# Kernel tuning notes

Measured on AMD Instinct MI355X. Metric: run time of the kernel, lower is better.

## Reference

```python
import jax, jax.numpy as jnp
import numpy as np

EPS = 1e-5
TEMPERATURE = 1.0


def _gn(x, w, b):
    # GroupNorm(dim, dim): num_groups == channels -> per-channel norm over spatial
    mu = x.mean((2, 3), keepdims=True)
    var = x.var((2, 3), keepdims=True)
    return (x - mu) * jax.lax.rsqrt(var + EPS) * w[None, :, None, None] + b[None, :, None, None]


def _deconv(x, w, b):
    # torch ConvTranspose2d(Cin, Cout, 3, stride=2, padding=1, output_padding=1)
    # == dilated conv with lhs_dilation=2, padding (1,2); kernel flip absorbed into random weights
    y = jax.lax.conv_general_dilated(
        x, w, window_strides=(1, 1), padding=((1, 2), (1, 2)),
        lhs_dilation=(2, 2), dimension_numbers=('NCHW', 'OIHW', 'NCHW'))
    return y + b[None, :, None, None]


def _spatial_softmax(logits, temp):
    # logits (..., h, w) -> expected (x, y) coords in [-1, 1], shape (..., 2)
    h, w = logits.shape[-2], logits.shape[-1]
    p = jax.nn.softmax(logits.reshape(*logits.shape[:-2], h * w) / temp, axis=-1)
    ys, xs = jnp.meshgrid(jnp.linspace(-1.0, 1.0, h), jnp.linspace(-1.0, 1.0, w), indexing='ij')
    ex = p @ xs.reshape(-1)
    ey = p @ ys.reshape(-1)
    return jnp.stack([ex, ey], axis=-1)


def setup_inputs() -> dict:
    key = jax.random.key(0)
    ks = iter(jax.random.split(key, 40))
    B, FC, FH = 512, 256, 4   # batch, encoder channels, encoder spatial
    H = 512                   # hidden_size
    STEPS, NHEADS, C = 5, 3, H // 8

    def nrm(shape, scale):
        return jax.random.normal(next(ks), shape, jnp.float32) * scale

    inp = {
        'feat': nrm((B, FC, FH, FH), 1.0),
        'action': jax.random.randint(next(ks), (B,), 0, NHEADS),
        'scene_idx': jax.random.randint(next(ks), (B,), 0, 10),
        'fc_w': nrm((FC, H), (2.0 / FC) ** 0.5),
        'fc_b': jnp.zeros((H,), jnp.float32),
    }
    for i, d in enumerate([512, 256, 128]):
        inp[f'gw{i}'] = jnp.ones((d,), jnp.float32)
        inp[f'gb{i}'] = jnp.zeros((d,), jnp.float32)
        inp[f'dw{i}'] = nrm((d // 2, d, 3, 3), (2.0 / (d * 9)) ** 0.5)
        inp[f'db{i}'] = jnp.zeros((d // 2,), jnp.float32)
    inp['hgw'] = jnp.ones((NHEADS, C), jnp.float32)
    inp['hgb'] = jnp.zeros((NHEADS, C), jnp.float32)
    inp['hcw'] = nrm((NHEADS, STEPS, C), (2.0 / C) ** 0.5)
    inp['hcb'] = jnp.zeros((NHEADS, STEPS), jnp.float32)
    return inp


def reference(feat, action, scene_idx, fc_w, fc_b,
              gw0, gb0, dw0, db0, gw1, gb1, dw1, db1, gw2, gb2, dw2, db2,
              hgw, hgb, hcw, hcb):
    # visual_fc1 applied channel-last == 1x1 linear over channels
    x = jax.nn.relu(jnp.einsum('bchw,cd->bdhw', feat, fc_w) + fc_b[None, :, None, None])
    # deconv stack: (B,512,4,4) -> (B,256,8,8) -> (B,128,16,16) -> (B,64,32,32)
    for gw, gb, dw, db in ((gw0, gb0, dw0, db0), (gw1, gb1, dw1, db1), (gw2, gb2, dw2, db2)):
        x = jax.nn.relu(_deconv(_gn(x, gw, gb), dw, db))
    # expert heads: shared per-channel normalization, head-specific affine fused into 1x1 conv
    mu = x.mean((2, 3), keepdims=True)
    var = x.var((2, 3), keepdims=True)
    xn = (x - mu) * jax.lax.rsqrt(var + EPS)                       # (B,64,32,32)
    w_eff = hcw * hgw[:, None, :]                                  # (A,S,C)
    b_eff = hcb + jnp.einsum('asc,ac->as', hcw, hgb)               # (A,S)
    logits = jnp.einsum('bchw,asc->abshw', xn, w_eff) + b_eff[:, None, :, None, None]
    coords = _spatial_softmax(logits, TEMPERATURE)                 # (A,B,S,2)
    # route each sample to its action's head (== masked scatter loop in torch)
    out = coords[action, jnp.arange(action.shape[0])]              # (B,S,2)
    return out
```

## Files before the change

### kernel.cpp

```cpp
#include <hip/hip_runtime.h>
#include <hip/hip_bf16.h>

#define DI __device__ __forceinline__
using u16 = unsigned short;
using u32 = unsigned int;

typedef short short8 __attribute__((ext_vector_type(8)));
typedef float f32x4 __attribute__((ext_vector_type(4)));

#define F4C(v, i) ((i) == 0 ? (v).x : (i) == 1 ? (v).y : (i) == 2 ? (v).z : (v).w)

DI float bflo(u32 u) { return __uint_as_float(u << 16); }
DI float bfhi(u32 u) { return __uint_as_float(u & 0xffff0000u); }
DI u16 f2bf(float a) {
  u32 xu = __float_as_uint(a);
  return (u16)((xu + 0x7fffu + ((xu >> 16) & 1)) >> 16);
}
DI u32 pack_bf16x2(float a, float b) {
  u32 xu = __float_as_uint(a), yu = __float_as_uint(b);
  xu = (xu + 0x7fffu + ((xu >> 16) & 1)) >> 16;
  yu = (yu + 0x7fffu + ((yu >> 16) & 1)) >> 16;
  return (xu & 0xffffu) | (yu << 16);
}

static constexpr size_t OFF_REGB = 0;
static constexpr size_t OFF_REGA = 16777216;
static constexpr size_t OFF_WT0  = 33554432;
static constexpr size_t OFF_WT1  = OFF_WT0 + 1179648;
static constexpr size_t OFF_WT2  = OFF_WT1 + 294912;
static constexpr size_t OFF_WTF  = OFF_WT2 + 73728;
static constexpr size_t OFF_ST   = 35200000;
static constexpr size_t O_PSUM = OFF_ST + 1048576;

__global__ __launch_bounds__(256)
void wtrans_all(const float* __restrict__ dw0, const float* __restrict__ dw1,
                const float* __restrict__ dw2, const float* __restrict__ fcw,
                u16* __restrict__ wt0, u16* __restrict__ wt1,
                u16* __restrict__ wt2, u16* __restrict__ wtf)
{
  int id = blockIdx.x * 256 + threadIdx.x;
  if (id < 131072) {
    int m = id >> 9, c = id & 511;
    const float* src = dw0 + ((size_t)m * 512 + c) * 9;
#pragma unroll
    for (int tap = 0; tap < 9; ++tap)
      wt0[((size_t)tap * 256 + m) * 512 + c] = f2bf(src[tap]);
  } else if (id < 163840) {
    int j = id - 131072;
    int m = j >> 8, c = j & 255;
    const float* src = dw1 + ((size_t)m * 256 + c) * 9;
#pragma unroll
    for (int tap = 0; tap < 9; ++tap)
      wt1[((size_t)tap * 128 + m) * 256 + c] = f2bf(src[tap]);
  } else if (id < 172032) {
    int j = id - 163840;
    int m = j >> 7, c = j & 127;
    const float* src = dw2 + ((size_t)m * 128 + c) * 9;
#pragma unroll
    for (int tap = 0; tap < 9; ++tap)
      wt2[((size_t)tap * 64 + m) * 128 + c] = f2bf(src[tap]);
  } else {
    int j = id - 172032;
    int d = j >> 8, c = j & 255;
    wtf[j] = f2bf(fcw[c * 512 + d]);
  }
}

DI void fc_stage_A(const float* __restrict__ feat, int b, u16* Ab, int t)
{
#pragma unroll
  for (int it = 0; it < 2; ++it) {
    int idx = t + it * 256;
    int cp = idx >> 2, hw4 = idx & 3;
    int c = cp * 2;
    const float* xp = feat + ((size_t)b * 256 + c) * 16 + hw4 * 4;
    float4 v0 = *(const float4*)xp;
    float4 v1 = *(const float4*)(xp + 16);
    int c64 = c >> 6, jb = (c & 63) >> 3;
#pragma unroll
    for (int j = 0; j < 4; ++j) {
      int hw = hw4 * 4 + j;
      int row = c64 * 16 + hw;
      *(u32*)&Ab[(row << 6) + ((jb ^ (row & 7)) << 3) + (c & 7)] =
          pack_bf16x2(F4C(v0, j), F4C(v1, j));
    }
  }
}

__global__ __launch_bounds__(256, 2)
void fc_mfma(const float* __restrict__ feat, const u16* __restrict__ wtf,
             const float* __restrict__ fb, const float* __restrict__ gw,
             const float* __restrict__ gb, u16* __restrict__ x0)
{
  __shared__ __align__(16) u16 Wl[256 * 64];
  __shared__ __align__(16) u16 Al[2][64 * 64];
  const int t = threadIdx.x;
  const int lane = t & 63, wave = t >> 6;
  const int n15 = lane & 15, kq = lane >> 4;
  const int d0 = blockIdx.x * 64;
  const int b0 = blockIdx.y * 8;

#pragma unroll
  for (int it = 0; it < 8; ++it) {
    int idx = t + it * 256;
    int dl = idx >> 5, jb32 = idx & 31;
    int row = (jb32 >> 3) * 64 + dl, jb = jb32 & 7;
    uint4 v = *(const uint4*)(wtf + (size_t)(d0 + dl) * 256 + jb32 * 8);
    *(uint4*)&Wl[(row << 6) + ((jb ^ (row & 7)) << 3)] = v;
  }
  fc_stage_A(feat, b0, Al[0], t);

  const int dg = d0 + wave * 16 + n15;
  const float bvn = fb[dg];
  const float gwv = gw[dg], gbv = gb[dg];

  for (int bi = 0; bi < 8; ++bi) {
    __syncthreads();
    if (bi + 1 < 8) fc_stage_A(feat, b0 + bi + 1, Al[(bi + 1) & 1], t);

    const u16* A = Al[bi & 1];
    f32x4 acc0 = {0.f, 0.f, 0.f, 0.f}, acc1 = {0.f, 0.f, 0.f, 0.f};
#pragma unroll
    for (int ks = 0; ks < 8; ++ks) {
      int js = ks * 4 + kq;
      int ra = (js >> 3) * 16 + n15;
      int rb = (js >> 3) * 64 + wave * 16 + n15;
      short8 av = *(const short8*)&A[(ra << 6) + (((js & 7) ^ (ra & 7)) << 3)];
      short8 bv = *(const short8*)&Wl[(rb << 6) + (((js & 7) ^ (rb & 7)) << 3)];
      if (ks & 1) acc1 = __builtin_amdgcn_mfma_f32_16x16x32_bf16(av, bv, acc1, 0, 0, 0);
      else        acc0 = __builtin_amdgcn_mfma_f32_16x16x32_bf16(av, bv, acc0, 0, 0, 0);
    }

    int b = b0 + bi;
    float v[4], s = 0.f, s2 = 0.f;
#pragma unroll
    for (int r = 0; r < 4; ++r) {
      v[r] = fmaxf(acc0[r] + acc1[r] + bvn, 0.f);
      s += v[r]; s2 += v[r] * v[r];
    }
    s  += __shfl_xor(s, 16, 64);  s  += __shfl_xor(s, 32, 64);
    s2 += __shfl_xor(s2, 16, 64); s2 += __shfl_xor(s2, 32, 64);
    float mu = s * (1.f / 16.f);
    float var = fmaxf(s2 * (1.f / 16.f) - mu * mu, 0.f);
    float scale = gwv * rsqrtf(var + 1e-5f);
    float shift = gbv - mu * scale;
#pragma unroll
    for (int r = 0; r < 4; ++r) v[r] = v[r] * scale + shift;
    uint2 pk = {pack_bf16x2(v[0], v[1]), pack_bf16x2(v[2], v[3])};
    *(uint2*)&x0[((size_t)b * 512 + dg) * 16 + kq * 4] = pk;
  }
}

template<int STAGE>
__global__ __launch_bounds__(256, 3)
void deconv_mfma(const u16* __restrict__ x, const u16* __restrict__ wt,
                 const float* __restrict__ bias, u16* __restrict__ y,
                 const float* __restrict__ gwn, const float* __restrict__ gbn)
{
  constexpr int CI  = STAGE == 0 ? 512 : 256;
  constexpr int CO  = CI / 2;
  constexpr int H   = STAGE == 0 ? 4 : 8;
  constexpr int S2I = H * H, S2O = 4 * S2I, W2 = 2 * H;
  constexpr int WP  = H + 1;
  constexpr int XROWS = STAGE == 0 ? 100 : 81;
  constexpr int NCH = CI / 64;
  __shared__ __align__(16) u16 Wl[288 * 64];
  __shared__ __align__(16) u16 Xl[XROWS * 64];
  __shared__ float2 sbuf[2][2][16];
  __shared__ float scl[32], shl[32];

  const int t = threadIdx.x;
  const int lane = t & 63, wave = t >> 6;
  const int ms = wave >> 1, ns = wave & 1;
  const int n15 = lane & 15, kq = lane >> 4;

  int m0, b0;
  m0 = blockIdx.x * 32; b0 = (STAGE == 0) ? blockIdx.y * 4 : blockIdx.y;

  int xrow[2];
#pragma unroll
  for (int ni = 0; ni < 2; ++ni) {
    if constexpr (STAGE == 0) xrow[ni] = (ns * 2 + ni) * 25 + (n15 >> 2) * 5 + (n15 & 3);
    else                      xrow[ni] = (2 * (ns * 2 + ni) + (n15 >> 3)) * 9 + (n15 & 7);
  }
  const int am = ms * 16 + n15;

  for (int i = t; i < XROWS * 32; i += 256) ((u32*)Xl)[i] = 0;

  f32x4 acc[2][4];
#pragma unroll
  for (int ni = 0; ni < 2; ++ni)
#pragma unroll
    for (int c = 0; c < 4; ++c) acc[ni][c] = f32x4{0.f, 0.f, 0.f, 0.f};

  for (int ch = 0; ch < NCH; ++ch) {
    const int c0 = ch * 64;
    __syncthreads();

#pragma unroll
    for (int it = 0; it < 9; ++it) {
      int idx = t + it * 256;
      int row = idx >> 3, jb = idx & 7;
      int tap = row >> 5, ml = row & 31;
      uint4 v = *(const uint4*)(wt + ((size_t)(tap * CO + m0 + ml)) * CI + c0 + jb * 8);
      *(uint4*)&Wl[(row << 6) + ((jb ^ (row & 7)) << 3)] = v;
    }

    for (int idx = t; idx < 16 * 32; idx += 256) {
      int q = idx & 15, p = idx >> 4;
      int c = c0 + 2 * p;
      int b, ldr, gpos;
      if constexpr (STAGE == 0) {
        int img = q >> 2, iy = q & 3;
        b = b0 + img; gpos = iy * 4; ldr = img * 25 + iy * 5;
      } else {
        int iy = q >> 1, cq = q & 1;
        b = b0; gpos = iy * 8 + cq * 4; ldr = iy * 9 + cq * 4;
      }
      const u16* xp = x + ((size_t)b * CI + c) * S2I + gpos;
      uint2 q0 = *(const uint2*)xp;
      uint2 q1 = *(const uint2*)(xp + S2I);
      int jb = p >> 2, sub = p & 3;
#pragma unroll
      for (int j = 0; j < 4; ++j) {
        int row = ldr + j;
        u32 w0 = (j < 2) ? q0.x : q0.y;
        u32 w1 = (j < 2) ? q1.x : q1.y;
        u32 lo = (j & 1) ? (w0 >> 16) : (w0 & 0xffffu);
        u32 hi = (j & 1) ? (w1 & 0xffff0000u) : (w1 << 16);
        *(u32*)&Xl[(row << 6) + ((jb ^ (row & 7)) << 3) + sub * 2] = lo | hi;
      }
    }
    __syncthreads();

#pragma unroll
    for (int s = 0; s < 2; ++s) {
      const int js = s * 4 + kq;
      short8 a[9];
#pragma unroll
      for (int tap = 0; tap < 9; ++tap) {
        int row = tap * 32 + am;
        a[tap] = *(const short8*)&Wl[(row << 6) + ((js ^ (row & 7)) << 3)];
      }
#pragma unroll
      for (int ni = 0; ni < 2; ++ni) {
        int r0 = xrow[ni], r1 = r0 + 1, r2 = r0 + WP, r3 = r0 + WP + 1;
        short8 b00 = *(const short8*)&Xl[(r0 << 6) + ((js ^ (r0 & 7)) << 3)];
        short8 b01 = *(const short8*)&Xl[(r1 << 6) + ((js ^ (r1 & 7)) << 3)];
        short8 b10 = *(const short8*)&Xl[(r2 << 6) + ((js ^ (r2 & 7)) << 3)];
        short8 b11 = *(const short8*)&Xl[(r3 << 6) + ((js ^ (r3 & 7)) << 3)];
        acc[ni][0] = __builtin_amdgcn_mfma_f32_16x16x32_bf16(a[4], b00, acc[ni][0], 0, 0, 0);
        acc[ni][1] = __builtin_amdgcn_mfma_f32_16x16x32_bf16(a[3], b00, acc[ni][1], 0, 0, 0);
        acc[ni][1] = __builtin_amdgcn_mfma_f32_16x16x32_bf16(a[5], b01, acc[ni][1], 0, 0, 0);
        acc[ni][2] = __builtin_amdgcn_mfma_f32_16x16x32_bf16(a[1], b00, acc[ni][2], 0, 0, 0);
        acc[ni][2] = __builtin_amdgcn_mfma_f32_16x16x32_bf16(a[7], b10, acc[ni][2], 0, 0, 0);
        acc[ni][3] = __builtin_amdgcn_mfma_f32_16x16x32_bf16(a[0], b00, acc[ni][3], 0, 0, 0);
        acc[ni][3] = __builtin_amdgcn_mfma_f32_16x16x32_bf16(a[2], b01, acc[ni][3], 0, 0, 0);
        acc[ni][3] = __builtin_amdgcn_mfma_f32_16x16x32_bf16(a[6], b10, acc[ni][3], 0, 0, 0);
        acc[ni][3] = __builtin_amdgcn_mfma_f32_16x16x32_bf16(a[8], b11, acc[ni][3], 0, 0, 0);
      }
    }
  }

  float bv[4];
#pragma unroll
  for (int r = 0; r < 4; ++r) bv[r] = bias[m0 + ms * 16 + kq * 4 + r];

  if constexpr (STAGE == 0) {
    float gw4[4], gb4[4];
#pragma unroll
    for (int r = 0; r < 4; ++r) {
      int m = m0 + ms * 16 + kq * 4 + r;
      gw4[r] = gwn[m]; gb4[r] = gbn[m];
    }
#pragma unroll
    for (int ni = 0; ni < 2; ++ni) {
      int b = b0 + ns * 2 + ni, iy = n15 >> 2, ix = n15 & 3;
      float val[4][4];
      float sr[4] = {0.f, 0.f, 0.f, 0.f}, sr2[4] = {0.f, 0.f, 0.f, 0.f};
#pragma unroll
      for (int cl = 0; cl < 4; ++cl)
#pragma unroll
        for (int r = 0; r < 4; ++r) {
          val[cl][r] = fmaxf(acc[ni][cl][r] + bv[r], 0.f);
          sr[r] += val[cl][r]; sr2[r] += val[cl][r] * val[cl][r];
        }
#pragma unroll
      for (int r = 0; r < 4; ++r) {
#pragma unroll
        for (int off = 1; off <= 8; off <<= 1) {
          sr[r]  += __shfl_xor(sr[r], off, 64);
          sr2[r] += __shfl_xor(sr2[r], off, 64);
        }
      }
      float scv[4], shv[4];
#pragma unroll
      for (int r = 0; r < 4; ++r) {
        float mu = sr[r] * (1.f / 64.f);
        float var = fmaxf(sr2[r] * (1.f / 64.f) - mu * mu, 0.f);
        scv[r] = gw4[r] * rsqrtf(var + 1e-5f);
        shv[r] = gb4[r] - mu * scv[r];
      }
#pragma unroll
      for (int r = 0; r < 4; ++r) {
        int m = m0 + ms * 16 + kq * 4 + r;
        size_t base = ((size_t)b * CO + m) * S2O + (size_t)(2 * iy) * W2 + 2 * ix;
        *(u32*)(y + base)      = pack_bf16x2(val[0][r] * scv[r] + shv[r],
                                             val[1][r] * scv[r] + shv[r]);
        *(u32*)(y + base + W2) = pack_bf16x2(val[2][r] * scv[r] + shv[r],
                                             val[3][r] * scv[r] + shv[r]);
      }
    }
  } else {
    float sr[4] = {0.f, 0.f, 0.f, 0.f}, sr2[4] = {0.f, 0.f, 0.f, 0.f};
#pragma unroll
    for (int ni = 0; ni < 2; ++ni)
#pragma unroll
      for (int cl = 0; cl < 4; ++cl)
#pragma unroll
        for (int r = 0; r < 4; ++r) {
          float v = fmaxf(acc[ni][cl][r] + bv[r], 0.f);
          sr[r] += v; sr2[r] += v * v;
        }
#pragma unroll
    for (int r = 0; r < 4; ++r) {
#pragma unroll
      for (int off = 1; off <= 8; off <<= 1) {
        sr[r]  += __shfl_xor(sr[r], off, 64);
        sr2[r] += __shfl_xor(sr2[r], off, 64);
      }
    }
    __syncthreads();
    if (n15 == 0) {
#pragma unroll
      for (int r = 0; r < 4; ++r) sbuf[ms][ns][kq * 4 + r] = float2{sr[r], sr2[r]};
    }
    __syncthreads();
    if (t < 32) {
      int msx = t >> 4, i = t & 15;
      float2 p0 = sbuf[msx][0][i], p1 = sbuf[msx][1][i];
      float s = p0.x + p1.x, s2 = p0.y + p1.y;
      float mu = s * (1.f / 256.f);
      float var = fmaxf(s2 * (1.f / 256.f) - mu * mu, 0.f);
      int m = m0 + msx * 16 + i;
      float scale = gwn[m] * rsqrtf(var + 1e-5f);
      scl[t] = scale;
      shl[t] = gbn[m] - mu * scale;
    }
    __syncthreads();
    float scv[4], shv[4];
#pragma unroll
    for (int r = 0; r < 4; ++r) {
      scv[r] = scl[ms * 16 + kq * 4 + r];
      shv[r] = shl[ms * 16 + kq * 4 + r];
    }
#pragma unroll
    for (int ni = 0; ni < 2; ++ni) {
      int iy = 2 * (ns * 2 + ni) + (n15 >> 3), ix = n15 & 7;
#pragma unroll
      for (int cl = 0; cl < 4; ++cl) {
        int opx = (2 * iy + (cl >> 1)) * 16 + 2 * ix + (cl & 1);
        size_t base = ((size_t)b0 * 256 + opx) * 128 + m0 + ms * 16 + kq * 4;
        float v0 = fmaxf(acc[ni][cl][0] + bv[0], 0.f) * scv[0] + shv[0];
        float v1 = fmaxf(acc[ni][cl][1] + bv[1], 0.f) * scv[1] + shv[1];
        float v2 = fmaxf(acc[ni][cl][2] + bv[2], 0.f) * scv[2] + shv[2];
        float v3 = fmaxf(acc[ni][cl][3] + bv[3], 0.f) * scv[3] + shv[3];
        *(u32*)(y + base)     = pack_bf16x2(v0, v1);
        *(u32*)(y + base + 2) = pack_bf16x2(v2, v3);
      }
    }
  }
}

#define XRD(row) (*(const short8*)&Xl[((row) << 6) + (((js ^ ((row) & 7))) << 3)])
__global__ __launch_bounds__(256, 2)
void deconv2_q(const u16* __restrict__ x, const u16* __restrict__ wt,
               const float* __restrict__ bias, u16* __restrict__ y,
               float2* __restrict__ psum)
{
  __shared__ __align__(16) u16 Wl[288 * 64];
  __shared__ __align__(16) u16 Xl[153 * 64];
  __shared__ float2 sbuf[2][2][16];

  const int t = threadIdx.x;
  const int lane = t & 63, wave = t >> 6;
  const int ms = wave >> 1, ns = wave & 1;
  const int n15 = lane & 15, kq = lane >> 4;
  const int m0  = (blockIdx.x & 1) * 32;
  const int qz2 = blockIdx.x >> 1;
  const int b   = blockIdx.y;

  for (int i = t; i < 153 * 32; i += 256) ((u32*)Xl)[i] = 0;

  const int am = ms * 16 + n15;
  const int xr0 = (ns * 4) * 17 + n15;

  f32x4 acc[4][4];
#pragma unroll
  for (int ni = 0; ni < 4; ++ni)
#pragma unroll
    for (int c = 0; c < 4; ++c) acc[ni][c] = f32x4{0.f, 0.f, 0.f, 0.f};

  const int NPX = (qz2 == 0) ? 144 : 128;
  for (int ch = 0; ch < 2; ++ch) {
    const int c0 = ch * 64;
    __syncthreads();

#pragma unroll
    for (int it = 0; it < 9; ++it) {
      int idx = t + it * 256;
      int row = idx >> 3, jb = idx & 7;
      int tap = row >> 5, ml = row & 31;
      uint4 v = *(const uint4*)(wt + ((size_t)(tap * 64 + m0 + ml)) * 128 + c0 + jb * 8);
      *(uint4*)&Wl[(row << 6) + ((jb ^ (row & 7)) << 3)] = v;
    }

    for (int idx = t; idx < NPX * 8; idx += 256) {
      int pxl = idx >> 3, jb = idx & 7;
      int rl = pxl >> 4, ix = pxl & 15;
      int gpx = (8 * qz2 + rl) * 16 + ix;
      uint4 q = *(const uint4*)(x + ((size_t)b * 256 + gpx) * 128 + c0 + jb * 8);
      int row = rl * 17 + ix;
      *(uint4*)&Xl[(row << 6) + ((jb ^ (row & 7)) << 3)] = q;
    }
    __syncthreads();

#pragma unroll
    for (int s = 0; s < 2; ++s) {
      const int js = s * 4 + kq;
      short8 a[9];
#pragma unroll
      for (int tap = 0; tap < 9; ++tap) {
        int row = tap * 32 + am;
        a[tap] = *(const short8*)&Wl[(row << 6) + ((js ^ (row & 7)) << 3)];
      }
      short8 Brow[10];
#pragma unroll
      for (int k = 0; k < 5; ++k) {
        Brow[2 * k]     = XRD(xr0 + 17 * k);
        Brow[2 * k + 1] = XRD(xr0 + 17 * k + 1);
      }
      __builtin_amdgcn_s_setprio(1);
#pragma unroll
      for (int ni = 0; ni < 4; ++ni) {
        short8 b00 = Brow[2 * ni],     b01 = Brow[2 * ni + 1];
        short8 b10 = Brow[2 * ni + 2], b11 = Brow[2 * ni + 3];
        acc[ni][0] = __builtin_amdgcn_mfma_f32_16x16x32_bf16(a[4], b00, acc[ni][0], 0, 0, 0);
        acc[ni][1] = __builtin_amdgcn_mfma_f32_16x16x32_bf16(a[3], b00, acc[ni][1], 0, 0, 0);
        acc[ni][1] = __builtin_amdgcn_mfma_f32_16x16x32_bf16(a[5], b01, acc[ni][1], 0, 0, 0);
        acc[ni][2] = __builtin_amdgcn_mfma_f32_16x16x32_bf16(a[1], b00, acc[ni][2], 0, 0, 0);
        acc[ni][2] = __builtin_amdgcn_mfma_f32_16x16x32_bf16(a[7], b10, acc[ni][2], 0, 0, 0);
        acc[ni][3] = __builtin_amdgcn_mfma_f32_16x16x32_bf16(a[0], b00, acc[ni][3], 0, 0, 0);
        acc[ni][3] = __builtin_amdgcn_mfma_f32_16x16x32_bf16(a[2], b01, acc[ni][3], 0, 0, 0);
        acc[ni][3] = __builtin_amdgcn_mfma_f32_16x16x32_bf16(a[6], b10, acc[ni][3], 0, 0, 0);
        acc[ni][3] = __builtin_amdgcn_mfma_f32_16x16x32_bf16(a[8], b11, acc[ni][3], 0, 0, 0);
      }
      __builtin_amdgcn_s_setprio(0);
    }
  }

  float bv[4];
#pragma unroll
  for (int r = 0; r < 4; ++r) bv[r] = bias[m0 + ms * 16 + kq * 4 + r];
  float sr[4] = {0.f, 0.f, 0.f, 0.f}, sr2[4] = {0.f, 0.f, 0.f, 0.f};
#pragma unroll
  for (int ni = 0; ni < 4; ++ni) {
    int iy = 8 * qz2 + ns * 4 + ni, ix = n15;
#pragma unroll
    for (int r = 0; r < 4; ++r) {
      int m = m0 + ms * 16 + kq * 4 + r;
      float v00 = fmaxf(acc[ni][0][r] + bv[r], 0.f);
      float v01 = fmaxf(acc[ni][1][r] + bv[r], 0.f);
      float v10 = fmaxf(acc[ni][2][r] + bv[r], 0.f);
      float v11 = fmaxf(acc[ni][3][r] + bv[r], 0.f);
      size_t base = ((size_t)b * 64 + m) * 1024 + (size_t)(2 * iy) * 32 + 2 * ix;
      *(u32*)(y + base)      = pack_bf16x2(v00, v01);
      *(u32*)(y + base + 32) = pack_bf16x2(v10, v11);
      sr[r]  += v00 + v01 + v10 + v11;
      sr2[r] += v00 * v00 + v01 * v01 + v10 * v10 + v11 * v11;
    }
  }
#pragma unroll
  for (int r = 0; r < 4; ++r) {
#pragma unroll
    for (int off = 1; off <= 8; off <<= 1) {
      sr[r]  += __shfl_xor(sr[r], off, 64);
      sr2[r] += __shfl_xor(sr2[r], off, 64);
    }
  }
  __syncthreads();
  if (n15 == 0) {
#pragma unroll
    for (int r = 0; r < 4; ++r) sbuf[ms][ns][kq * 4 + r] = float2{sr[r], sr2[r]};
  }
  __syncthreads();
  if (t < 32) {
    int msx = t >> 4, i = t & 15;
    float2 p0 = sbuf[msx][0][i], p1 = sbuf[msx][1][i];
    int m = m0 + msx * 16 + i;
    psum[((size_t)b * 64 + m) * 2 + qz2] = float2{p0.x + p1.x, p0.y + p1.y};
  }
}

DI float breduce_sum(float v, float* buf) {
#pragma unroll
  for (int off = 32; off; off >>= 1) v += __shfl_xor(v, off, 64);
  if ((threadIdx.x & 63) == 0) buf[threadIdx.x >> 6] = v;
  __syncthreads();
  float r = (buf[0] + buf[1]) + (buf[2] + buf[3]);
  __syncthreads();
  return r;
}
DI float breduce_max(float v, float* buf) {
#pragma unroll
  for (int off = 32; off; off >>= 1) v = fmaxf(v, __shfl_xor(v, off, 64));
  if ((threadIdx.x & 63) == 0) buf[threadIdx.x >> 6] = v;
  __syncthreads();
  float r = fmaxf(fmaxf(buf[0], buf[1]), fmaxf(buf[2], buf[3]));
  __syncthreads();
  return r;
}

__global__ __launch_bounds__(256)
void head_kernel(const u16* __restrict__ x3, const float2* __restrict__ psum,
                 const int* __restrict__ action, const float* __restrict__ hgw,
                 const float* __restrict__ hcw, float* __restrict__ out)
{
  constexpr int C = 64, S = 5, P = 1024;
  const int b = blockIdx.x, t = threadIdx.x;
  const int a = action[b];
  __shared__ float weff[S * C];
  __shared__ float sc_l[C], sh_l[C];
  __shared__ float rbuf[4];
  if (t < C) {
    float2 p0 = psum[((size_t)b * C + t) * 2 + 0];
    float2 p1 = psum[((size_t)b * C + t) * 2 + 1];
    float s = p0.x + p1.x, s2 = p0.y + p1.y;
    float mu = s * (1.f / 1024.f);
    float var = fmaxf(s2 * (1.f / 1024.f) - mu * mu, 0.f);
    float rstd = rsqrtf(var + 1e-5f);
    sc_l[t] = rstd; sh_l[t] = -mu * rstd;
  }
  for (int j = t; j < S * C; j += 256) {
    int s = j >> 6, c = j & 63;
    weff[j] = hcw[(a * S + s) * C + c] * hgw[a * C + c];
  }
  __syncthreads();

  float L[S][4];
#pragma unroll
  for (int s = 0; s < S; ++s)
#pragma unroll
    for (int k = 0; k < 4; ++k) L[s][k] = 0.f;

  const u32* xb = (const u32*)(x3 + (size_t)b * C * P);
  for (int c = 0; c < C; ++c) {
    float scv = sc_l[c], shv = sh_l[c];
    u32 u0 = xb[c * 512 + t];
    u32 u1 = xb[c * 512 + t + 256];
    float xv[4] = {bflo(u0) * scv + shv, bfhi(u0) * scv + shv,
                   bflo(u1) * scv + shv, bfhi(u1) * scv + shv};
#pragma unroll
    for (int s = 0; s < S; ++s) {
      float wv = weff[s * C + c];
#pragma unroll
      for (int k = 0; k < 4; ++k) L[s][k] += xv[k] * wv;
    }
  }

#pragma unroll
  for (int s = 0; s < S; ++s) {
    float m = fmaxf(fmaxf(L[s][0], L[s][1]), fmaxf(L[s][2], L[s][3]));
    m = breduce_max(m, rbuf);
    float se = 0.f, sx = 0.f, sy = 0.f;
    const int pix[4] = {2 * t, 2 * t + 1, 512 + 2 * t, 512 + 2 * t + 1};
#pragma unroll
    for (int k = 0; k < 4; ++k) {
      int p = pix[k];
      float e = __expf(L[s][k] - m);
      se += e;
      sx += e * ((float)(p & 31) * (2.f / 31.f) - 1.f);
      sy += e * ((float)(p >> 5) * (2.f / 31.f) - 1.f);
    }
    se = breduce_sum(se, rbuf);
    sx = breduce_sum(sx, rbuf);
    sy = breduce_sum(sy, rbuf);
    if (t == 0) {
      out[(b * S + s) * 2 + 0] = sx / se;
      out[(b * S + s) * 2 + 1] = sy / se;
    }
  }
}

extern "C" void kernel_launch(void* const* d_in, const int* in_sizes, int n_in,
                              void* d_out, int out_size, void* d_ws, size_t ws_size,
                              hipStream_t stream)
{
  (void)in_sizes; (void)n_in; (void)out_size; (void)ws_size;
  const float* feat   = (const float*)d_in[0];
  const int*   action = (const int*)d_in[1];
  const float* fc_w = (const float*)d_in[3];
  const float* fc_b = (const float*)d_in[4];
  const float* gw0  = (const float*)d_in[5];
  const float* gb0  = (const float*)d_in[6];
  const float* dw0  = (const float*)d_in[7];
  const float* db0  = (const float*)d_in[8];
  const float* gw1  = (const float*)d_in[9];
  const float* gb1  = (const float*)d_in[10];
  const float* dw1  = (const float*)d_in[11];
  const float* db1  = (const float*)d_in[12];
  const float* gw2  = (const float*)d_in[13];
  const float* gb2  = (const float*)d_in[14];
  const float* dw2  = (const float*)d_in[15];
  const float* db2  = (const float*)d_in[16];
  const float* hgw  = (const float*)d_in[17];
  const float* hcw  = (const float*)d_in[19];

  float* ws = (float*)d_ws;
  u16* x0 = (u16*)(ws + OFF_REGB);
  u16* x2 = (u16*)(ws + OFF_REGB);
  u16* x1 = (u16*)(ws + OFF_REGA);
  u16* x3 = (u16*)(ws + OFF_REGA);
  u16* wt0 = (u16*)(ws + OFF_WT0);
  u16* wt1 = (u16*)(ws + OFF_WT1);
  u16* wt2 = (u16*)(ws + OFF_WT2);
  u16* wtf = (u16*)(ws + OFF_WTF);
  float2* psum = (float2*)(ws + O_PSUM);

  wtrans_all<<<1184, 256, 0, stream>>>(dw0, dw1, dw2, fc_w, wt0, wt1, wt2, wtf);
  fc_mfma<<<dim3(8, 64), 256, 0, stream>>>(feat, wtf, fc_b, gw0, gb0, x0);
  deconv_mfma<0><<<dim3(8, 128), 256, 0, stream>>>(x0, wt0, db0, x1, gw1, gb1);
  deconv_mfma<1><<<dim3(4, 512), 256, 0, stream>>>(x1, wt1, db1, x2, gw2, gb2);
  deconv2_q<<<dim3(4, 512), 256, 0, stream>>>(x2, wt2, db2, x3, psum);
  head_kernel<<<512, 256, 0, stream>>>(x3, psum, action, hgw, hcw, (float*)d_out);
}
```

Before: 253.6 us.

## Use channel-last intermediate between deconv stages and remap blocks per XCD

Stage-0 deconv now writes its GroupNorm'd output channel-last (NHWC), so stage 1 can stage its input tile into LDS with contiguous 16-byte vector loads instead of strided 8-byte gathers and bit shuffling. All kernels also remap the linear block index so that blocks working on the same batch range land on the same XCD (lin & 7). This is meant to improve L2 locality for shared weights and activations. The risks are less coalesced stores from stage 0, since each 8-byte store now lands at a different pixel, and a layout contract between the two stages that both must keep in sync.

```diff
diff --git a/kernel.cpp b/kernel.cpp
--- a/kernel.cpp
+++ b/kernel.cpp
@@ -97,8 +97,10 @@
   const int t = threadIdx.x;
   const int lane = t & 63, wave = t >> 6;
   const int n15 = lane & 15, kq = lane >> 4;
-  const int d0 = blockIdx.x * 64;
-  const int b0 = blockIdx.y * 8;
+  const int lin = blockIdx.y * 8 + blockIdx.x;
+  const int xk = lin & 7, pos = lin >> 3;
+  const int d0 = (pos & 7) * 64;
+  const int b0 = (xk * 8 + (pos >> 3)) * 8;
 
 #pragma unroll
   for (int it = 0; it < 8; ++it) {
@@ -160,7 +162,7 @@
   constexpr int CI  = STAGE == 0 ? 512 : 256;
   constexpr int CO  = CI / 2;
   constexpr int H   = STAGE == 0 ? 4 : 8;
-  constexpr int S2I = H * H, S2O = 4 * S2I, W2 = 2 * H;
+  constexpr int S2I = H * H;
   constexpr int WP  = H + 1;
   constexpr int XROWS = STAGE == 0 ? 100 : 81;
   constexpr int NCH = CI / 64;
@@ -175,7 +177,17 @@
   const int n15 = lane & 15, kq = lane >> 4;
 
   int m0, b0;
-  m0 = blockIdx.x * 32; b0 = (STAGE == 0) ? blockIdx.y * 4 : blockIdx.y;
+  if constexpr (STAGE == 0) {
+    int lin = blockIdx.y * 8 + blockIdx.x;
+    int xk = lin & 7, pos = lin >> 3;
+    m0 = (pos & 7) * 32;
+    b0 = (xk * 16 + (pos >> 3)) * 4;
+  } else {
+    int lin = blockIdx.y * 4 + blockIdx.x;
+    int xk = lin & 7, pos = lin >> 3;
+    m0 = (pos & 3) * 32;
+    b0 = xk * 64 + (pos >> 2);
+  }
 
   int xrow[2];
 #pragma unroll
@@ -206,29 +218,33 @@
       *(uint4*)&Wl[(row << 6) + ((jb ^ (row & 7)) << 3)] = v;
     }
 
-    for (int idx = t; idx < 16 * 32; idx += 256) {
-      int q = idx & 15, p = idx >> 4;
-      int c = c0 + 2 * p;
-      int b, ldr, gpos;
-      if constexpr (STAGE == 0) {
+    if constexpr (STAGE == 0) {
+      for (int idx = t; idx < 16 * 32; idx += 256) {
+        int q = idx & 15, p = idx >> 4;
+        int c = c0 + 2 * p;
         int img = q >> 2, iy = q & 3;
-        b = b0 + img; gpos = iy * 4; ldr = img * 25 + iy * 5;
-      } else {
-        int iy = q >> 1, cq = q & 1;
-        b = b0; gpos = iy * 8 + cq * 4; ldr = iy * 9 + cq * 4;
-      }
-      const u16* xp = x + ((size_t)b * CI + c) * S2I + gpos;
-      uint2 q0 = *(const uint2*)xp;
-      uint2 q1 = *(const uint2*)(xp + S2I);
-      int jb = p >> 2, sub = p & 3;
-#pragma unroll
-      for (int j = 0; j < 4; ++j) {
-        int row = ldr + j;
-        u32 w0 = (j < 2) ? q0.x : q0.y;
-        u32 w1 = (j < 2) ? q1.x : q1.y;
-        u32 lo = (j & 1) ? (w0 >> 16) : (w0 & 0xffffu);
-        u32 hi = (j & 1) ? (w1 & 0xffff0000u) : (w1 << 16);
-        *(u32*)&Xl[(row << 6) + ((jb ^ (row & 7)) << 3) + sub * 2] = lo | hi;
+        int b = b0 + img, gpos = iy * 4, ldr = img * 25 + iy * 5;
+        const u16* xp = x + ((size_t)b * CI + c) * S2I + gpos;
+        uint2 q0 = *(const uint2*)xp;
+        uint2 q1 = *(const uint2*)(xp + S2I);
+        int jb = p >> 2, sub = p & 3;
+#pragma unroll
+        for (int j = 0; j < 4; ++j) {
+          int row = ldr + j;
+          u32 w0 = (j < 2) ? q0.x : q0.y;
+          u32 w1 = (j < 2) ? q1.x : q1.y;
+          u32 lo = (j & 1) ? (w0 >> 16) : (w0 & 0xffffu);
+          u32 hi = (j & 1) ? (w1 & 0xffff0000u) : (w1 << 16);
+          *(u32*)&Xl[(row << 6) + ((jb ^ (row & 7)) << 3) + sub * 2] = lo | hi;
+        }
+      }
+    } else {
+      for (int idx = t; idx < 64 * 8; idx += 256) {
+        int pxl = idx >> 3, jb = idx & 7;
+        int py = pxl >> 3, px_ = pxl & 7;
+        uint4 q = *(const uint4*)(x + ((size_t)b0 * 64 + pxl) * 256 + c0 + jb * 8);
+        int row = py * 9 + px_;
+        *(uint4*)&Xl[(row << 6) + ((jb ^ (row & 7)) << 3)] = q;
       }
     }
     __syncthreads();
@@ -302,13 +318,14 @@
         shv[r] = gb4[r] - mu * scv[r];
       }
 #pragma unroll
-      for (int r = 0; r < 4; ++r) {
-        int m = m0 + ms * 16 + kq * 4 + r;
-        size_t base = ((size_t)b * CO + m) * S2O + (size_t)(2 * iy) * W2 + 2 * ix;
-        *(u32*)(y + base)      = pack_bf16x2(val[0][r] * scv[r] + shv[r],
-                                             val[1][r] * scv[r] + shv[r]);
-        *(u32*)(y + base + W2) = pack_bf16x2(val[2][r] * scv[r] + shv[r],
-                                             val[3][r] * scv[r] + shv[r]);
+      for (int cl = 0; cl < 4; ++cl) {
+        int oy = 2 * iy + (cl >> 1), ox = 2 * ix + (cl & 1);
+        size_t base = ((size_t)b * 64 + oy * 8 + ox) * 256 + m0 + ms * 16 + kq * 4;
+        uint2 pk = {pack_bf16x2(val[cl][0] * scv[0] + shv[0],
+                                val[cl][1] * scv[1] + shv[1]),
+                    pack_bf16x2(val[cl][2] * scv[2] + shv[2],
+                                val[cl][3] * scv[3] + shv[3])};
+        *(uint2*)(y + base) = pk;
       }
     }
   } else {
@@ -386,9 +403,11 @@
   const int lane = t & 63, wave = t >> 6;
   const int ms = wave >> 1, ns = wave & 1;
   const int n15 = lane & 15, kq = lane >> 4;
-  const int m0  = (blockIdx.x & 1) * 32;
-  const int qz2 = blockIdx.x >> 1;
-  const int b   = blockIdx.y;
+  const int lin = blockIdx.y * 4 + blockIdx.x;
+  const int xk = lin & 7, pos = lin >> 3;
+  const int b   = xk * 64 + (pos >> 2);
+  const int m0  = (pos & 1) * 32;
+  const int qz2 = (pos >> 1) & 1;
 
   for (int i = t; i < 153 * 32; i += 256) ((u32*)Xl)[i] = 0;
 
@@ -527,7 +546,8 @@
                  const float* __restrict__ hcw, float* __restrict__ out)
 {
   constexpr int C = 64, S = 5, P = 1024;
-  const int b = blockIdx.x, t = threadIdx.x;
+  const int t = threadIdx.x;
+  const int b = (blockIdx.x & 7) * 64 + (blockIdx.x >> 3);
   const int a = action[b];
   __shared__ float weff[S * C];
   __shared__ float sc_l[C], sh_l[C];
```

Result: faster. 244.8 us (-3.4%).
